# Performance work log

Hardware: AMD Instinct MI355X
Metric: run time of the kernel (lower is better)

## Reference

```python
import jax, jax.numpy as jnp
import numpy as np

B, Q, K, H = 16, 512, 512, 64
DQ, DK, DV = 256, 256, 256
MASK_VAL = -1000000.0


def setup_inputs() -> dict:
    key = jax.random.key(0)
    ks = jax.random.split(key, 7)
    queries = jax.random.normal(ks[0], (B, Q, DQ), dtype=jnp.float32)
    keys = jax.random.normal(ks[1], (B, K, DK), dtype=jnp.float32)
    values = jax.random.normal(ks[2], (B, K, DV), dtype=jnp.float32)
    valid_lens = jax.random.randint(ks[3], (B,), 1, K + 1).astype(jnp.int32)
    # learned params (nn.Linear, bias=False): weight shape [out, in]
    Wq = jax.random.normal(ks[4], (H, DQ), dtype=jnp.float32) / np.sqrt(DQ)
    Wk = jax.random.normal(ks[5], (H, DK), dtype=jnp.float32) / np.sqrt(DK)
    wv = jax.random.normal(ks[6], (H,), dtype=jnp.float32) / np.sqrt(H)
    return {"queries": queries, "keys": keys, "values": values,
            "valid_lens": valid_lens, "Wq": Wq, "Wk": Wk, "wv": wv}


def reference(queries, keys, values, valid_lens, Wq, Wk, wv):
    q = jnp.einsum('bqd,hd->bqh', queries, Wq)          # [B,Q,H]
    k = jnp.einsum('bkd,hd->bkh', keys, Wk)             # [B,K,H]
    feats = jnp.tanh(q[:, :, None, :] + k[:, None, :, :])  # [B,Q,K,H]
    scores = jnp.einsum('bqkh,h->bqk', feats, wv)       # [B,Q,K]
    kmask = jnp.arange(K)[None, None, :] < valid_lens[:, None, None]
    scores = jnp.where(kmask, scores, MASK_VAL)
    attn = jax.nn.softmax(scores, axis=-1)              # [B,Q,K]
    return jnp.einsum('bqk,bkv->bqv', attn, values)     # [B,Q,DV]
```

## Files before the change

### kernel.cpp

```cpp
#include <hip/hip_runtime.h>
#include <math.h>

#if defined(__has_builtin)
#  if __has_builtin(__builtin_amdgcn_exp2f)
#    define EXP2F(x) __builtin_amdgcn_exp2f(x)
#  endif
#  if __has_builtin(__builtin_amdgcn_rcpf)
#    define RCPF(x) __builtin_amdgcn_rcpf(x)
#  endif
#endif
#ifndef EXP2F
#  define EXP2F(x) exp2f(x)
#endif
#ifndef RCPF
#  define RCPF(x) (1.0f/(x))
#endif

static constexpr int Bn = 16, QN = 512, KN = 512, Hn = 64, DV = 256, DIN = 256;
static constexpr int TQ = 8;
static constexpr int PR = 32;
static constexpr float TWO_LOG2E = 2.8853900817779268f;
static constexpr float LOG2E     = 1.4426950408889634f;

__global__ __launch_bounds__(256) void proj_kernel(
    const float* __restrict__ queries, const float* __restrict__ keys,
    const float* __restrict__ Wq, const float* __restrict__ Wk,
    float* __restrict__ qe, float* __restrict__ ekT)
{
  __shared__ __align__(16) float xs[PR][36];
  int blk = blockIdx.x;
  bool is_k = blk >= 256;
  int tile = is_k ? blk - 256 : blk;
  const float* X = is_k ? keys : queries;
  const float* W = is_k ? Wk : Wq;
  int row0 = tile * PR;
  int t = threadIdx.x;
  int c = t & 63;
  int wg = t >> 6;
  float acc[8];
  #pragma unroll
  for (int i = 0; i < 8; ++i) acc[i] = 0.f;

  for (int dc = 0; dc < DIN; dc += 32) {
    __syncthreads();
    {
      int row = t >> 3, dp = t & 7;
      float4 v = *(const float4*)(X + (size_t)(row0 + row) * DIN + dc + dp * 4);
      *(float4*)&xs[row][dp * 4] = v;
    }
    __syncthreads();
    const float* wr = W + c * DIN + dc;
    #pragma unroll
    for (int dd = 0; dd < 32; dd += 4) {
      float4 w4 = *(const float4*)(wr + dd);
      #pragma unroll
      for (int i = 0; i < 8; ++i) {
        float4 x4 = *(const float4*)&xs[wg * 8 + i][dd];
        acc[i] += w4.x * x4.x + w4.y * x4.y + w4.z * x4.z + w4.w * x4.w;
      }
    }
  }
  #pragma unroll
  for (int i = 0; i < 8; ++i) {
    int row = row0 + wg * 8 + i;
    float e = EXP2F(acc[i] * TWO_LOG2E);
    if (!is_k) {
      qe[(size_t)row * Hn + c] = e;
    } else {
      int b = row >> 9, k = row & (KN - 1);
      ekT[((size_t)b * Hn + c) * KN + k] = e;
    }
  }
}

__global__ __launch_bounds__(512) void attn_kernel(
    const float* __restrict__ qe,
    const float* __restrict__ ekT,
    const float* __restrict__ values,
    const int*   __restrict__ valid_lens,
    const float* __restrict__ wv,
    float* __restrict__ out)
{
  __shared__ __align__(16) float qes[TQ * Hn];
  __shared__ float wv2[Hn];
  __shared__ __align__(16) float pt[KN][12];
  __shared__ float wsum[8][8];
  __shared__ float inv_s[TQ];
  __shared__ __align__(16) float pacc[TQ][DV];

  int t = threadIdx.x;
  int b = blockIdx.x & 15;
  int q0 = (blockIdx.x >> 4) * TQ;
  int L = valid_lens[b];
  int lane = t & 63, wave = t >> 6;

  qes[t] = qe[((size_t)b * QN + q0) * Hn + t];
  if (t < Hn) wv2[t] = 2.0f * wv[t];
  __syncthreads();

  float S = 0.f;
  #pragma unroll
  for (int h = 0; h < Hn; ++h) S += wv2[h];
  S *= 0.5f;

  {
    int k = t;
    float sc[TQ];
    #pragma unroll
    for (int r = 0; r < TQ; ++r) sc[r] = S;
    if (k < L) {
      const float* kp = ekT + (size_t)b * Hn * KN + k;
      #pragma unroll 4
      for (int h = 0; h < Hn; ++h) {
        float ek = kp[(size_t)h * KN];
        float w2 = wv2[h];
        #pragma unroll
        for (int r = 0; r < TQ; ++r) {
          float d = qes[r * Hn + h] * ek + 1.0f;
          sc[r] -= w2 * RCPF(d);
        }
      }
    }
    float p[TQ];
    #pragma unroll
    for (int r = 0; r < TQ; ++r) p[r] = (k < L) ? EXP2F(sc[r] * LOG2E) : 0.f;
    if (k < L) {
      *(float4*)&pt[k][0] = make_float4(p[0], p[1], p[2], p[3]);
      *(float4*)&pt[k][4] = make_float4(p[4], p[5], p[6], p[7]);
    }
    #pragma unroll
    for (int r = 0; r < TQ; ++r) {
      float s = p[r];
      #pragma unroll
      for (int off = 32; off > 0; off >>= 1) s += __shfl_xor(s, off, 64);
      if (lane == r) wsum[wave][r] = s;
    }
  }
  __syncthreads();
  if (t < TQ) {
    float s = 0.f;
    #pragma unroll
    for (int w = 0; w < 8; ++w) s += wsum[w][t];
    inv_s[t] = 1.0f / s;
  }
  __syncthreads();

  int col = t & (DV - 1), half = t >> 8;
  int mid = L >> 1;
  int k0 = half ? mid : 0;
  int k1 = half ? L : mid;
  float acc[TQ];
  #pragma unroll
  for (int r = 0; r < TQ; ++r) acc[r] = 0.f;
  const float* vb = values + (size_t)b * KN * DV + col;
  #pragma unroll 4
  for (int k = k0; k < k1; ++k) {
    float val = vb[(size_t)k * DV];
    float4 pa = *(const float4*)&pt[k][0];
    float4 pb = *(const float4*)&pt[k][4];
    acc[0] += pa.x * val; acc[1] += pa.y * val;
    acc[2] += pa.z * val; acc[3] += pa.w * val;
    acc[4] += pb.x * val; acc[5] += pb.y * val;
    acc[6] += pb.z * val; acc[7] += pb.w * val;
  }
  if (half) {
    #pragma unroll
    for (int r = 0; r < TQ; ++r) pacc[r][col] = acc[r];
  }
  __syncthreads();
  if (!half) {
    float* ob = out + ((size_t)b * QN + q0) * DV + col;
    #pragma unroll
    for (int r = 0; r < TQ; ++r)
      ob[(size_t)r * DV] = (acc[r] + pacc[r][col]) * inv_s[r];
  }
}

extern "C" void kernel_launch(void* const* d_in, const int* in_sizes, int n_in,
                              void* d_out, int out_size, void* d_ws, size_t ws_size,
                              hipStream_t stream) {
  const float* queries    = (const float*)d_in[0];
  const float* keys       = (const float*)d_in[1];
  const float* values     = (const float*)d_in[2];
  const int*   valid_lens = (const int*)d_in[3];
  const float* Wq         = (const float*)d_in[4];
  const float* Wk         = (const float*)d_in[5];
  const float* wv         = (const float*)d_in[6];
  float* out = (float*)d_out;

  float* qe  = (float*)d_ws;
  float* ekT = qe + (size_t)Bn * QN * Hn;

  proj_kernel<<<512, 256, 0, stream>>>(queries, keys, Wq, Wk, qe, ekT);
  attn_kernel<<<Bn * (QN / TQ), 512, 0, stream>>>(qe, ekT, values,
                                                  valid_lens, wv, out);
}
```

Before: 156.9 us.

## Transpose q projection output, restructure proj tiling, split PV over four key quarters

The projection kernel now gives each thread one row and eight heads, using wave-uniform weight loads and larger 64x128 input tiles, and writes both q and k exponentials transposed (head-major). The attention kernel reads the q exponentials directly from global memory (uniform across the block) instead of staging them in LDS. It also maps blocks batch-major so consecutive blocks share the same batch's keys and values. The PV stage splits keys into four quarters with float2 column pairs and reduces three partials through LDS, which aims to shorten the serial k loop at the cost of more shared memory and reduction work.

```diff
diff --git a/kernel.cpp b/kernel.cpp
--- a/kernel.cpp
+++ b/kernel.cpp
@@ -18,90 +18,81 @@
 
 static constexpr int Bn = 16, QN = 512, KN = 512, Hn = 64, DV = 256, DIN = 256;
 static constexpr int TQ = 8;
-static constexpr int PR = 32;
 static constexpr float TWO_LOG2E = 2.8853900817779268f;
 static constexpr float LOG2E     = 1.4426950408889634f;
 
-__global__ __launch_bounds__(256) void proj_kernel(
+__global__ __launch_bounds__(512) void proj_kernel(
     const float* __restrict__ queries, const float* __restrict__ keys,
     const float* __restrict__ Wq, const float* __restrict__ Wk,
-    float* __restrict__ qe, float* __restrict__ ekT)
+    float* __restrict__ qeT, float* __restrict__ ekT)
 {
-  __shared__ __align__(16) float xs[PR][36];
+  __shared__ __align__(16) float xs[64][132];
+  int t = threadIdx.x;
   int blk = blockIdx.x;
-  bool is_k = blk >= 256;
-  int tile = is_k ? blk - 256 : blk;
+  bool is_k = blk >= 128;
+  int tile = blk & 127;
   const float* X = is_k ? keys : queries;
   const float* W = is_k ? Wk : Wq;
-  int row0 = tile * PR;
-  int t = threadIdx.x;
-  int c = t & 63;
-  int wg = t >> 6;
+  int row0 = tile * 64;
+  int lane = t & 63;
+  int w8 = __builtin_amdgcn_readfirstlane(t >> 6);
+  const float* Wb = W + (size_t)w8 * 8 * DIN;
   float acc[8];
   #pragma unroll
-  for (int i = 0; i < 8; ++i) acc[i] = 0.f;
-
-  for (int dc = 0; dc < DIN; dc += 32) {
+  for (int j = 0; j < 8; ++j) acc[j] = 0.f;
+
+  #pragma unroll
+  for (int kc = 0; kc < 2; ++kc) {
     __syncthreads();
-    {
-      int row = t >> 3, dp = t & 7;
-      float4 v = *(const float4*)(X + (size_t)(row0 + row) * DIN + dc + dp * 4);
-      *(float4*)&xs[row][dp * 4] = v;
+    #pragma unroll
+    for (int j = 0; j < 4; ++j) {
+      int idx = t + 512 * j;
+      int row = idx >> 5, c4 = idx & 31;
+      *(float4*)&xs[row][c4 * 4] =
+          *(const float4*)(X + (size_t)(row0 + row) * DIN + kc * 128 + c4 * 4);
     }
     __syncthreads();
-    const float* wr = W + c * DIN + dc;
-    #pragma unroll
-    for (int dd = 0; dd < 32; dd += 4) {
-      float4 w4 = *(const float4*)(wr + dd);
+    const float* Wc = Wb + kc * 128;
+    #pragma unroll 4
+    for (int kq = 0; kq < 32; ++kq) {
+      float4 x4 = *(const float4*)&xs[lane][kq * 4];
       #pragma unroll
-      for (int i = 0; i < 8; ++i) {
-        float4 x4 = *(const float4*)&xs[wg * 8 + i][dd];
-        acc[i] += w4.x * x4.x + w4.y * x4.y + w4.z * x4.z + w4.w * x4.w;
+      for (int j = 0; j < 8; ++j) {
+        float4 w4 = *(const float4*)(Wc + j * DIN + kq * 4);
+        acc[j] += x4.x * w4.x + x4.y * w4.y + x4.z * w4.z + x4.w * w4.w;
       }
     }
   }
-  #pragma unroll
-  for (int i = 0; i < 8; ++i) {
-    int row = row0 + wg * 8 + i;
-    float e = EXP2F(acc[i] * TWO_LOG2E);
-    if (!is_k) {
-      qe[(size_t)row * Hn + c] = e;
-    } else {
-      int b = row >> 9, k = row & (KN - 1);
-      ekT[((size_t)b * Hn + c) * KN + k] = e;
-    }
-  }
+  int row = row0 + lane;
+  int b = row >> 9, rk = row & (KN - 1);
+  float* outp = is_k ? ekT : qeT;
+  #pragma unroll
+  for (int j = 0; j < 8; ++j)
+    outp[((size_t)b * Hn + w8 * 8 + j) * KN + rk] = EXP2F(acc[j] * TWO_LOG2E);
 }
 
 __global__ __launch_bounds__(512) void attn_kernel(
-    const float* __restrict__ qe,
+    const float* __restrict__ qeT,
     const float* __restrict__ ekT,
     const float* __restrict__ values,
     const int*   __restrict__ valid_lens,
     const float* __restrict__ wv,
     float* __restrict__ out)
 {
-  __shared__ __align__(16) float qes[TQ * Hn];
-  __shared__ float wv2[Hn];
   __shared__ __align__(16) float pt[KN][12];
-  __shared__ float wsum[8][8];
+  __shared__ __align__(16) float pacc[3][TQ][DV];
+  __shared__ float wsum[8][TQ];
   __shared__ float inv_s[TQ];
-  __shared__ __align__(16) float pacc[TQ][DV];
 
   int t = threadIdx.x;
-  int b = blockIdx.x & 15;
-  int q0 = (blockIdx.x >> 4) * TQ;
+  int b = blockIdx.x >> 6;
+  int q0 = (blockIdx.x & 63) * TQ;
   int L = valid_lens[b];
   int lane = t & 63, wave = t >> 6;
 
-  qes[t] = qe[((size_t)b * QN + q0) * Hn + t];
-  if (t < Hn) wv2[t] = 2.0f * wv[t];
-  __syncthreads();
-
   float S = 0.f;
   #pragma unroll
-  for (int h = 0; h < Hn; ++h) S += wv2[h];
-  S *= 0.5f;
+  for (int h = 0; h < Hn; ++h) S += wv[h];
 
   {
     int k = t;
@@ -109,14 +100,16 @@
     #pragma unroll
     for (int r = 0; r < TQ; ++r) sc[r] = S;
     if (k < L) {
-      const float* kp = ekT + (size_t)b * Hn * KN + k;
-      #pragma unroll 4
+      const float* qbase = qeT + (size_t)b * Hn * QN + q0;
+      const float* kbase = ekT + (size_t)b * Hn * KN + k;
+      #pragma unroll 2
       for (int h = 0; h < Hn; ++h) {
-        float ek = kp[(size_t)h * KN];
-        float w2 = wv2[h];
+        float ek = kbase[(size_t)h * KN];
+        const float* qp = qbase + (size_t)h * QN;
+        float w2 = 2.0f * wv[h];
         #pragma unroll
         for (int r = 0; r < TQ; ++r) {
-          float d = qes[r * Hn + h] * ek + 1.0f;
+          float d = qp[r] * ek + 1.0f;
           sc[r] -= w2 * RCPF(d);
         }
       }
@@ -145,34 +138,46 @@
   }
   __syncthreads();
 
-  int col = t & (DV - 1), half = t >> 8;
-  int mid = L >> 1;
-  int k0 = half ? mid : 0;
-  int k1 = half ? L : mid;
-  float acc[TQ];
-  #pragma unroll
-  for (int r = 0; r < TQ; ++r) acc[r] = 0.f;
-  const float* vb = values + (size_t)b * KN * DV + col;
-  #pragma unroll 4
+  int p2 = t & 127, kq = t >> 7;
+  int c = p2 * 2;
+  int k0 = (L * kq) >> 2, k1 = (L * (kq + 1)) >> 2;
+  float a0[TQ], a1[TQ];
+  #pragma unroll
+  for (int r = 0; r < TQ; ++r) { a0[r] = 0.f; a1[r] = 0.f; }
+  const float* vb = values + (size_t)b * KN * DV + c;
+  #pragma unroll 2
   for (int k = k0; k < k1; ++k) {
-    float val = vb[(size_t)k * DV];
+    float2 v2 = *(const float2*)(vb + (size_t)k * DV);
     float4 pa = *(const float4*)&pt[k][0];
     float4 pb = *(const float4*)&pt[k][4];
-    acc[0] += pa.x * val; acc[1] += pa.y * val;
-    acc[2] += pa.z * val; acc[3] += pa.w * val;
-    acc[4] += pb.x * val; acc[5] += pb.y * val;
-    acc[6] += pb.z * val; acc[7] += pb.w * val;
-  }
-  if (half) {
-    #pragma unroll
-    for (int r = 0; r < TQ; ++r) pacc[r][col] = acc[r];
+    a0[0] += pa.x * v2.x; a1[0] += pa.x * v2.y;
+    a0[1] += pa.y * v2.x; a1[1] += pa.y * v2.y;
+    a0[2] += pa.z * v2.x; a1[2] += pa.z * v2.y;
+    a0[3] += pa.w * v2.x; a1[3] += pa.w * v2.y;
+    a0[4] += pb.x * v2.x; a1[4] += pb.x * v2.y;
+    a0[5] += pb.y * v2.x; a1[5] += pb.y * v2.y;
+    a0[6] += pb.z * v2.x; a1[6] += pb.z * v2.y;
+    a0[7] += pb.w * v2.x; a1[7] += pb.w * v2.y;
+  }
+  if (kq) {
+    #pragma unroll
+    for (int r = 0; r < TQ; ++r)
+      *(float2*)&pacc[kq - 1][r][c] = make_float2(a0[r], a1[r]);
   }
   __syncthreads();
-  if (!half) {
-    float* ob = out + ((size_t)b * QN + q0) * DV + col;
-    #pragma unroll
-    for (int r = 0; r < TQ; ++r)
-      ob[(size_t)r * DV] = (acc[r] + pacc[r][col]) * inv_s[r];
+  if (kq == 0) {
+    float* ob = out + ((size_t)b * QN + q0) * DV + c;
+    #pragma unroll
+    for (int r = 0; r < TQ; ++r) {
+      float s0 = a0[r], s1 = a1[r];
+      #pragma unroll
+      for (int q = 0; q < 3; ++q) {
+        float2 pp = *(const float2*)&pacc[q][r][c];
+        s0 += pp.x; s1 += pp.y;
+      }
+      float iv = inv_s[r];
+      *(float2*)(ob + (size_t)r * DV) = make_float2(s0 * iv, s1 * iv);
+    }
   }
 }
 
@@ -188,10 +193,10 @@
   const float* wv         = (const float*)d_in[6];
   float* out = (float*)d_out;
 
-  float* qe  = (float*)d_ws;
-  float* ekT = qe + (size_t)Bn * QN * Hn;
-
-  proj_kernel<<<512, 256, 0, stream>>>(queries, keys, Wq, Wk, qe, ekT);
-  attn_kernel<<<Bn * (QN / TQ), 512, 0, stream>>>(qe, ekT, values,
+  float* qeT = (float*)d_ws;
+  float* ekT = qeT + (size_t)Bn * Hn * QN;
+
+  proj_kernel<<<256, 512, 0, stream>>>(queries, keys, Wq, Wk, qeT, ekT);
+  attn_kernel<<<Bn * (QN / TQ), 512, 0, stream>>>(qeT, ekT, values,
                                                   valid_lens, wv, out);
 }
```

Result: faster. 150.3 us (-4.2%).

## Sort batches by valid length, repack projection weights, restructure proj and attention kernels

Applied to the files above, without the earlier changes.

Adds a prep kernel that repacks Wq/Wk into an h-interleaved layout, and rewrites the projection kernel so each thread reads x rows directly from global memory instead of staging them through shared memory. Key outputs are now transposed through shared memory so stores are coalesced. A new order kernel sorts batches by valid length so the longest blocks are scheduled first, aiming to reduce tail imbalance. The attention kernel transposes the cached q features for float4 LDS reads and removes one barrier. Two extra tiny launches add overhead and use more workspace.

```diff
diff --git a/kernel.cpp b/kernel.cpp
--- a/kernel.cpp
+++ b/kernel.cpp
@@ -18,59 +18,92 @@
 
 static constexpr int Bn = 16, QN = 512, KN = 512, Hn = 64, DV = 256, DIN = 256;
 static constexpr int TQ = 8;
-static constexpr int PR = 32;
+static constexpr int NTASK = Bn * (QN / TQ);
 static constexpr float TWO_LOG2E = 2.8853900817779268f;
 static constexpr float LOG2E     = 1.4426950408889634f;
 
+__global__ __launch_bounds__(256) void prep_kernel(
+    const float* __restrict__ Wq, const float* __restrict__ Wk,
+    float* __restrict__ wpq, float* __restrict__ wpk)
+{
+  int i = blockIdx.x * 256 + threadIdx.x;
+  int k2 = i >> 6, h = i & 63;
+  wpq[i * 2 + 0] = Wq[h * DIN + 2 * k2];
+  wpq[i * 2 + 1] = Wq[h * DIN + 2 * k2 + 1];
+  wpk[i * 2 + 0] = Wk[h * DIN + 2 * k2];
+  wpk[i * 2 + 1] = Wk[h * DIN + 2 * k2 + 1];
+}
+
 __global__ __launch_bounds__(256) void proj_kernel(
     const float* __restrict__ queries, const float* __restrict__ keys,
-    const float* __restrict__ Wq, const float* __restrict__ Wk,
+    const float* __restrict__ wpq, const float* __restrict__ wpk,
     float* __restrict__ qe, float* __restrict__ ekT)
 {
-  __shared__ __align__(16) float xs[PR][36];
-  int blk = blockIdx.x;
-  bool is_k = blk >= 256;
-  int tile = is_k ? blk - 256 : blk;
-  const float* X = is_k ? keys : queries;
-  const float* W = is_k ? Wk : Wq;
-  int row0 = tile * PR;
+  __shared__ float tr[Hn][17];
   int t = threadIdx.x;
-  int c = t & 63;
-  int wg = t >> 6;
-  float acc[8];
-  #pragma unroll
-  for (int i = 0; i < 8; ++i) acc[i] = 0.f;
-
-  for (int dc = 0; dc < DIN; dc += 32) {
+  int h = t & 63;
+  int w4 = __builtin_amdgcn_readfirstlane(t >> 6);
+  bool is_k = blockIdx.x >= 512;
+  int tile = blockIdx.x & 511;
+  const float* X  = is_k ? keys : queries;
+  const float* Wp = is_k ? wpk : wpq;
+  int row0 = tile * 16 + w4 * 4;
+  const float* x0 = X + (size_t)row0 * DIN;
+
+  float a0 = 0.f, a1 = 0.f, a2 = 0.f, a3 = 0.f;
+  #pragma unroll 4
+  for (int c = 0; c < 32; ++c) {
+    float2 wa = *(const float2*)(Wp + ((size_t)(4 * c + 0) * Hn + h) * 2);
+    float2 wb = *(const float2*)(Wp + ((size_t)(4 * c + 1) * Hn + h) * 2);
+    float2 wc = *(const float2*)(Wp + ((size_t)(4 * c + 2) * Hn + h) * 2);
+    float2 wd = *(const float2*)(Wp + ((size_t)(4 * c + 3) * Hn + h) * 2);
+    #pragma unroll
+    for (int j = 0; j < 4; ++j) {
+      float4 xa = *(const float4*)(x0 + (size_t)j * DIN + c * 8);
+      float4 xb = *(const float4*)(x0 + (size_t)j * DIN + c * 8 + 4);
+      float s = xa.x * wa.x + xa.y * wa.y + xa.z * wb.x + xa.w * wb.y
+              + xb.x * wc.x + xb.y * wc.y + xb.z * wd.x + xb.w * wd.y;
+      if (j == 0) a0 += s; else if (j == 1) a1 += s;
+      else if (j == 2) a2 += s; else a3 += s;
+    }
+  }
+  float e[4] = {EXP2F(a0 * TWO_LOG2E), EXP2F(a1 * TWO_LOG2E),
+                EXP2F(a2 * TWO_LOG2E), EXP2F(a3 * TWO_LOG2E)};
+  if (!is_k) {
+    #pragma unroll
+    for (int j = 0; j < 4; ++j)
+      qe[(size_t)(row0 + j) * Hn + h] = e[j];
+  } else {
+    #pragma unroll
+    for (int j = 0; j < 4; ++j) tr[h][w4 * 4 + j] = e[j];
     __syncthreads();
-    {
-      int row = t >> 3, dp = t & 7;
-      float4 v = *(const float4*)(X + (size_t)(row0 + row) * DIN + dc + dp * 4);
-      *(float4*)&xs[row][dp * 4] = v;
-    }
-    __syncthreads();
-    const float* wr = W + c * DIN + dc;
-    #pragma unroll
-    for (int dd = 0; dd < 32; dd += 4) {
-      float4 w4 = *(const float4*)(wr + dd);
-      #pragma unroll
-      for (int i = 0; i < 8; ++i) {
-        float4 x4 = *(const float4*)&xs[wg * 8 + i][dd];
-        acc[i] += w4.x * x4.x + w4.y * x4.y + w4.z * x4.z + w4.w * x4.w;
-      }
-    }
-  }
-  #pragma unroll
-  for (int i = 0; i < 8; ++i) {
-    int row = row0 + wg * 8 + i;
-    float e = EXP2F(acc[i] * TWO_LOG2E);
-    if (!is_k) {
-      qe[(size_t)row * Hn + c] = e;
-    } else {
-      int b = row >> 9, k = row & (KN - 1);
-      ekT[((size_t)b * Hn + c) * KN + k] = e;
-    }
-  }
+    int h2 = t >> 2, kk = t & 3;
+    int krow = tile * 16;
+    int b = krow >> 9, k0 = (krow & (KN - 1)) + kk * 4;
+    float4 v = make_float4(tr[h2][kk * 4], tr[h2][kk * 4 + 1],
+                           tr[h2][kk * 4 + 2], tr[h2][kk * 4 + 3]);
+    *(float4*)(ekT + ((size_t)b * Hn + h2) * KN + k0) = v;
+  }
+}
+
+__global__ void order_kernel(const int* __restrict__ valid_lens,
+                             int* __restrict__ order)
+{
+  int t = threadIdx.x;
+  __shared__ int batch_at[Bn];
+  if (t < Bn) {
+    int L = valid_lens[t];
+    int r = 0;
+    #pragma unroll
+    for (int b2 = 0; b2 < Bn; ++b2) {
+      int L2 = valid_lens[b2];
+      if (L2 > L || (L2 == L && b2 < t)) ++r;
+    }
+    batch_at[r] = t;
+  }
+  __syncthreads();
+  for (int i = t; i < NTASK; i += 256)
+    order[i] = batch_at[i >> 6] * 64 + (i & 63);
 }
 
 __global__ __launch_bounds__(512) void attn_kernel(
@@ -79,62 +112,76 @@
     const float* __restrict__ values,
     const int*   __restrict__ valid_lens,
     const float* __restrict__ wv,
+    const int*   __restrict__ order,
     float* __restrict__ out)
 {
-  __shared__ __align__(16) float qes[TQ * Hn];
-  __shared__ float wv2[Hn];
+  __shared__ __align__(16) float qes2[Hn][TQ];
   __shared__ __align__(16) float pt[KN][12];
-  __shared__ float wsum[8][8];
+  __shared__ __align__(16) float pacc[TQ][DV];
+  __shared__ float wsum[8][TQ];
   __shared__ float inv_s[TQ];
-  __shared__ __align__(16) float pacc[TQ][DV];
 
   int t = threadIdx.x;
-  int b = blockIdx.x & 15;
-  int q0 = (blockIdx.x >> 4) * TQ;
+  int task = order[blockIdx.x];
+  int b = task >> 6;
+  int q0 = (task & 63) * TQ;
   int L = valid_lens[b];
   int lane = t & 63, wave = t >> 6;
 
-  qes[t] = qe[((size_t)b * QN + q0) * Hn + t];
-  if (t < Hn) wv2[t] = 2.0f * wv[t];
+  qes2[t >> 3][t & 7] = qe[(size_t)(b * QN + q0 + (t & 7)) * Hn + (t >> 3)];
   __syncthreads();
 
   float S = 0.f;
   #pragma unroll
-  for (int h = 0; h < Hn; ++h) S += wv2[h];
-  S *= 0.5f;
-
+  for (int h = 0; h < Hn; ++h) S += wv[h];
+
+  float rowsum[TQ];
   {
     int k = t;
-    float sc[TQ];
-    #pragma unroll
-    for (int r = 0; r < TQ; ++r) sc[r] = S;
+    float p[TQ];
     if (k < L) {
-      const float* kp = ekT + (size_t)b * Hn * KN + k;
-      #pragma unroll 4
-      for (int h = 0; h < Hn; ++h) {
-        float ek = kp[(size_t)h * KN];
-        float w2 = wv2[h];
+      float sc[TQ];
+      #pragma unroll
+      for (int r = 0; r < TQ; ++r) sc[r] = S;
+      const float* kb = ekT + (size_t)b * Hn * KN + k;
+      for (int h0 = 0; h0 < Hn; h0 += 8) {
+        float ekv[8];
         #pragma unroll
-        for (int r = 0; r < TQ; ++r) {
-          float d = qes[r * Hn + h] * ek + 1.0f;
-          sc[r] -= w2 * RCPF(d);
+        for (int j = 0; j < 8; ++j)
+          ekv[j] = kb[(size_t)(h0 + j) * KN];
+        #pragma unroll
+        for (int j = 0; j < 8; ++j) {
+          int h = h0 + j;
+          float w2 = 2.0f * wv[h];
+          float4 qa = *(const float4*)&qes2[h][0];
+          float4 qb = *(const float4*)&qes2[h][4];
+          float ek = ekv[j];
+          sc[0] -= w2 * RCPF(qa.x * ek + 1.0f);
+          sc[1] -= w2 * RCPF(qa.y * ek + 1.0f);
+          sc[2] -= w2 * RCPF(qa.z * ek + 1.0f);
+          sc[3] -= w2 * RCPF(qa.w * ek + 1.0f);
+          sc[4] -= w2 * RCPF(qb.x * ek + 1.0f);
+          sc[5] -= w2 * RCPF(qb.y * ek + 1.0f);
+          sc[6] -= w2 * RCPF(qb.z * ek + 1.0f);
+          sc[7] -= w2 * RCPF(qb.w * ek + 1.0f);
         }
       }
-    }
-    float p[TQ];
-    #pragma unroll
-    for (int r = 0; r < TQ; ++r) p[r] = (k < L) ? EXP2F(sc[r] * LOG2E) : 0.f;
-    if (k < L) {
+      #pragma unroll
+      for (int r = 0; r < TQ; ++r) p[r] = EXP2F(sc[r] * LOG2E);
       *(float4*)&pt[k][0] = make_float4(p[0], p[1], p[2], p[3]);
       *(float4*)&pt[k][4] = make_float4(p[4], p[5], p[6], p[7]);
+    } else {
+      #pragma unroll
+      for (int r = 0; r < TQ; ++r) p[r] = 0.f;
     }
     #pragma unroll
     for (int r = 0; r < TQ; ++r) {
       float s = p[r];
       #pragma unroll
       for (int off = 32; off > 0; off >>= 1) s += __shfl_xor(s, off, 64);
-      if (lane == r) wsum[wave][r] = s;
-    }
+      rowsum[r] = s;
+    }
+    if (lane < TQ) wsum[wave][lane] = rowsum[lane];
   }
   __syncthreads();
   if (t < TQ) {
@@ -143,16 +190,15 @@
     for (int w = 0; w < 8; ++w) s += wsum[w][t];
     inv_s[t] = 1.0f / s;
   }
-  __syncthreads();
-
-  int col = t & (DV - 1), half = t >> 8;
+
+  int c = t & (DV - 1), half = t >> 8;
   int mid = L >> 1;
   int k0 = half ? mid : 0;
   int k1 = half ? L : mid;
   float acc[TQ];
   #pragma unroll
   for (int r = 0; r < TQ; ++r) acc[r] = 0.f;
-  const float* vb = values + (size_t)b * KN * DV + col;
+  const float* vb = values + (size_t)b * KN * DV + c;
   #pragma unroll 4
   for (int k = k0; k < k1; ++k) {
     float val = vb[(size_t)k * DV];
@@ -165,14 +211,14 @@
   }
   if (half) {
     #pragma unroll
-    for (int r = 0; r < TQ; ++r) pacc[r][col] = acc[r];
+    for (int r = 0; r < TQ; ++r) pacc[r][c] = acc[r];
   }
   __syncthreads();
   if (!half) {
-    float* ob = out + ((size_t)b * QN + q0) * DV + col;
+    float* ob = out + (size_t)(b * QN + q0) * DV + c;
     #pragma unroll
     for (int r = 0; r < TQ; ++r)
-      ob[(size_t)r * DV] = (acc[r] + pacc[r][col]) * inv_s[r];
+      ob[(size_t)r * DV] = (acc[r] + pacc[r][c]) * inv_s[r];
   }
 }
 
@@ -188,10 +234,16 @@
   const float* wv         = (const float*)d_in[6];
   float* out = (float*)d_out;
 
-  float* qe  = (float*)d_ws;
+  char* ws = (char*)d_ws;
+  float* qe  = (float*)ws;
   float* ekT = qe + (size_t)Bn * QN * Hn;
-
-  proj_kernel<<<512, 256, 0, stream>>>(queries, keys, Wq, Wk, qe, ekT);
-  attn_kernel<<<Bn * (QN / TQ), 512, 0, stream>>>(qe, ekT, values,
-                                                  valid_lens, wv, out);
-}
+  float* wpq = ekT + (size_t)Bn * Hn * KN;
+  float* wpk = wpq + Hn * DIN;
+  int* order = (int*)(wpk + Hn * DIN);
+
+  prep_kernel<<<32, 256, 0, stream>>>(Wq, Wk, wpq, wpk);
+  order_kernel<<<1, 256, 0, stream>>>(valid_lens, order);
+  proj_kernel<<<1024, 256, 0, stream>>>(queries, keys, wpq, wpk, qe, ekT);
+  attn_kernel<<<NTASK, 512, 0, stream>>>(qe, ekT, values, valid_lens, wv,
+                                         order, out);
+}
```

Result: faster. 149.6 us (-4.7%).
